# Kernel tuning notes

Measured on AMD Instinct MI355X. Metric: run time of the kernel, lower is better.

The kernel has to match this reference:

```python
import jax, jax.numpy as jnp
import numpy as np

T = 0.2          # temperature
W = 0.1          # loss weight
BIG = 2 ** 30    # sentinel label for masked-out samples


def setup_inputs() -> dict:
    key = jax.random.key(0)
    k1, k2, k3, k4 = jax.random.split(key, 4)
    bs, C, Gn, S = 32, 128, 256, 16
    grouped_features = jax.random.normal(k1, (bs, C, Gn, S), dtype=jnp.float32)
    # instance labels in [-1, 8): -1 = background
    proposal_instance_mask = jax.random.randint(k2, (bs, Gn, S), -1, 8, dtype=jnp.int32)
    # seed indices with duplicates possible (range 40 over 16 samples)
    grouped_indices = jax.random.randint(k3, (bs, Gn, S), 0, 40, dtype=jnp.int32)
    context_compen = jax.random.normal(k4, (1, C), dtype=jnp.float32)
    return {
        "proposal_instance_mask": proposal_instance_mask,
        "grouped_features": grouped_features,
        "grouped_indices": grouped_indices,
        "context_compen": context_compen,
    }


def _group_loss(feat, idx, lab, ctx):
    # feat: [S, C], idx: [S], lab: [S], ctx: [C]
    # NOTE: sum_{a,b} f_a . g_b / (n_f * n_g) == mean(f) . mean(g), so the
    # original tiny-mm contrastive loss reduces to pairwise dots of per-instance means.
    S, C = feat.shape
    pos = jnp.arange(S)
    # unique count of seed indices -> truncate to first u samples (as in torch code)
    si = jnp.sort(idx)
    u = 1 + jnp.sum(si[1:] != si[:-1])
    valid = pos < u
    lab_m = jnp.where(valid, lab, BIG)
    # per-group unique labels (sorted), jit-friendly
    sl = jnp.sort(lab_m)
    new = jnp.concatenate([jnp.ones((1,), bool), sl[1:] != sl[:-1]])
    cid = jnp.cumsum(new) - 1                      # compact id of each sorted label
    uniq = jnp.full((S,), BIG, sl.dtype).at[cid].set(sl)
    n_labels = jnp.sum(new & (sl != BIG))          # number of distinct valid labels
    has_bg = uniq[0] == -1                         # -1 sorts first if present
    # per-instance mean features via segment scatter-add
    comp = jnp.searchsorted(uniq, lab_m)           # sample -> compact instance slot
    sums = jnp.zeros((S, C), feat.dtype).at[comp].add(jnp.where(valid[:, None], feat, 0.0))
    cnts = jnp.zeros((S,), feat.dtype).at[comp].add(valid.astype(feat.dtype))
    means = sums / jnp.maximum(cnts, 1.0)[:, None]
    hb = has_bg.astype(jnp.int32)
    fg_count = n_labels - hb
    inst_num = fg_count + 1                        # bg slot always present
    # row 0 = bg mean (or context_compen if no bg), rows 1.. = fg means
    gidx = jnp.clip(pos + hb - 1, 0, S - 1)
    M = means[gidx]
    M = M.at[0].set(jnp.where(has_bg, M[0], ctx))
    inst_valid = pos < inst_num
    sim = (M @ M.T) / T                            # [S, S] tiny matmul of means
    sim_m = jnp.where(inst_valid[None, :], sim, -jnp.inf)
    lse = jax.scipy.special.logsumexp(sim_m, axis=1)
    li = lse - jnp.diagonal(sim)                   # -log(pos/(pos+neg)) per fg row
    fg_mask = inst_valid & (pos >= 1)
    gl = jnp.sum(jnp.where(fg_mask, li, 0.0)) / jnp.maximum(inst_num - 1, 1).astype(feat.dtype)
    return gl, fg_count >= 1


def reference(proposal_instance_mask, grouped_features, grouped_indices, context_compen):
    bs, C, Gn, S = grouped_features.shape
    feats = grouped_features.transpose(0, 2, 3, 1).reshape(-1, S, C)  # [G, S, C]
    idxs = grouped_indices.reshape(-1, S)
    labs = proposal_instance_mask.reshape(-1, S)
    ctx = context_compen[0]
    gl, gv = jax.vmap(lambda f, i, l: _group_loss(f, i, l, ctx))(feats, idxs, labs)
    gvf = gv.astype(gl.dtype)
    return jnp.sum(gl * gvf) / jnp.sum(gvf) * W
```

## Files before the change

### kernel.cpp

```cpp
#include <hip/hip_runtime.h>

#define GQ    8192
#define BLKG  8
#define MROW  132
#define SQRT5 2.23606797749978969f

template<int CTRL>
__device__ __forceinline__ float dpp_add(float v) {
    int t = __builtin_amdgcn_update_dpp(0, __float_as_int(v), CTRL, 0xF, 0xF, true);
    return v + __int_as_float(t);
}
__device__ __forceinline__ float wave_sum64(float v) {
    v = dpp_add<0x111>(v);
    v = dpp_add<0x112>(v);
    v = dpp_add<0x114>(v);
    v = dpp_add<0x118>(v);
    v = dpp_add<0x142>(v);
    v = dpp_add<0x143>(v);
    return v;
}

__global__ __launch_bounds__(64 * BLKG, 4) void group_loss_kernel(
    const int*   __restrict__ labs,
    const float* __restrict__ feats,
    const int*   __restrict__ idxs,
    const float* __restrict__ ctx,
    float2* __restrict__ ws)
{
    __shared__ float SH[128 * MROW];

    const int l  = threadIdx.x & 63;
    const int w  = threadIdx.x >> 6;
    const int g0 = blockIdx.x * BLKG;
    const int g  = g0 + w;
    const int b  = g0 >> 8;
    const int gn0 = g0 & 255;

    int myidx = -1, mylab = -2;
    if (l < 16) { myidx = idxs[g * 16 + l]; mylab = labs[g * 16 + l]; }
    const float cx0 = ctx[l], cx1 = ctx[l + 64];

    {
        const int half = l >> 5;
        const int lo   = l & 31;
        const float* base = feats + (long)b * 524288 + (long)gn0 * 16;
        #pragma unroll
        for (int k = 0; k < 8; ++k) {
            const int c = k * 16 + w * 2 + half;
            const float4 v = *(const float4*)(base + (long)c * 4096 + lo * 4);
            *(float4*)(SH + c * MROW + lo * 4) = v;
        }
    }
    __syncthreads();

    unsigned long long mm = ~0ull;
    #pragma unroll
    for (int bit = 0; bit < 6; ++bit) {
        const unsigned long long bb = __ballot((myidx >> bit) & 1);
        mm &= ((myidx >> bit) & 1) ? bb : ~bb;
    }
    const bool dup = (mm & ((1ull << l) - 1) & 0xFFFFull) != 0ull;
    const int u = __popcll(__ballot((l < 16) && !dup));

    const bool valid = l < u;
    const int bid = valid ? (mylab + 1) : 255;

    int cnt[9];
    #pragma unroll
    for (int r = 0; r < 9; ++r) cnt[r] = __popcll(__ballot(bid == r));
    const bool has_bg = cnt[0] > 0;
    int fg_count = 0, pm = 0;
    #pragma unroll
    for (int r = 1; r < 9; ++r)
        if (cnt[r] > 0) { ++fg_count; pm |= 1 << r; }

    float fa[16], fb[16];
    {
        const float* Ra = SH + l * MROW + w * 16;
        const float* Rb = SH + (l + 64) * MROW + w * 16;
        #pragma unroll
        for (int q = 0; q < 4; ++q) {
            const float4 x = *(const float4*)(Ra + 4 * q);
            const float4 y = *(const float4*)(Rb + 4 * q);
            fa[4*q+0] = x.x; fa[4*q+1] = x.y; fa[4*q+2] = x.z; fa[4*q+3] = x.w;
            fb[4*q+0] = y.x; fb[4*q+1] = y.y; fb[4*q+2] = y.z; fb[4*q+3] = y.w;
        }
    }

    float m0[9] = {0,0,0,0,0,0,0,0,0};
    float m1[9] = {0,0,0,0,0,0,0,0,0};
    #pragma unroll
    for (int s = 0; s < 16; ++s) {
        if (s < u) {
            const int bs = __builtin_amdgcn_readlane(bid, s);
            switch (bs) {
                case 0: m0[0] += fa[s]; m1[0] += fb[s]; break;
                case 1: m0[1] += fa[s]; m1[1] += fb[s]; break;
                case 2: m0[2] += fa[s]; m1[2] += fb[s]; break;
                case 3: m0[3] += fa[s]; m1[3] += fb[s]; break;
                case 4: m0[4] += fa[s]; m1[4] += fb[s]; break;
                case 5: m0[5] += fa[s]; m1[5] += fb[s]; break;
                case 6: m0[6] += fa[s]; m1[6] += fb[s]; break;
                case 7: m0[7] += fa[s]; m1[7] += fb[s]; break;
                case 8: m0[8] += fa[s]; m1[8] += fb[s]; break;
            }
        }
    }
    #pragma unroll
    for (int r = 0; r < 9; ++r) {
        const float sc = SQRT5 / (float)(cnt[r] > 0 ? cnt[r] : 1);
        m0[r] *= sc; m1[r] *= sc;
    }
    if (!has_bg) { m0[0] = cx0 * SQRT5; m1[0] = cx1 * SQRT5; }

    const int PI_[44] = {1,1, 2,2,2, 3,3,3,3, 4,4,4,4,4, 5,5,5,5,5,5,
                         6,6,6,6,6,6,6, 7,7,7,7,7,7,7,7, 8,8,8,8,8,8,8,8,8};
    const int PJ_[44] = {0,1, 0,1,2, 0,1,2,3, 0,1,2,3,4, 0,1,2,3,4,5,
                         0,1,2,3,4,5,6, 0,1,2,3,4,5,6,7, 0,1,2,3,4,5,6,7,8};
    const int cm = pm | 1;
    int svi[44];
    #pragma unroll
    for (int k = 0; k < 44; ++k) {
        float pv = m0[PI_[k]] * m0[PJ_[k]] + m1[PI_[k]] * m1[PJ_[k]];
        pv = wave_sum64(pv);
        const int s = __builtin_amdgcn_readlane(__float_as_int(pv), 63);
        const bool keep = (((cm >> PI_[k]) & 1) != 0) && (((cm >> PJ_[k]) & 1) != 0);
        svi[k] = keep ? s : 0xFF800000;
    }
    const int OFF_[9] = {0, 0, 2, 5, 9, 14, 20, 27, 35};
    #define SK(i, j) __int_as_float(svi[((i) >= (j)) ? (OFF_[(i)] + (j)) : (OFF_[(j)] + (i))])

    float ssum = 0.0f;
    #pragma unroll
    for (int r = 1; r < 9; ++r) {
        if ((pm >> r) & 1) {
            float vmax = SK(r, 0);
            #pragma unroll
            for (int j = 1; j < 9; ++j) vmax = fmaxf(vmax, SK(r, j));
            float se = 0.0f;
            #pragma unroll
            for (int j = 0; j < 9; ++j) se += __expf(SK(r, j) - vmax);
            ssum += vmax + __logf(se) - SK(r, r);
        }
    }
    #undef SK

    if (l == 0) {
        float2 r;
        r.x = ssum / (float)(fg_count > 0 ? fg_count : 1);
        r.y = (fg_count > 0) ? 1.0f : 0.0f;
        ws[g] = r;
    }
}

__global__ __launch_bounds__(1024) void reduce_kernel(
    const float2* __restrict__ ws, float* __restrict__ out)
{
    __shared__ float sa[1024], sb[1024];
    const int t = threadIdx.x;
    float a = 0.0f, b2 = 0.0f;
    for (int g = t; g < GQ; g += 1024) {
        float2 v = ws[g];
        a += v.x; b2 += v.y;
    }
    sa[t] = a; sb[t] = b2;
    __syncthreads();
    for (int off = 512; off > 0; off >>= 1) {
        if (t < off) { sa[t] += sa[t + off]; sb[t] += sb[t + off]; }
        __syncthreads();
    }
    if (t == 0) out[0] = 0.1f * (sa[0] / sb[0]);
}

extern "C" void kernel_launch(void* const* d_in, const int* in_sizes, int n_in,
                              void* d_out, int out_size, void* d_ws, size_t ws_size,
                              hipStream_t stream) {
    const int*   labs  = (const int*)d_in[0];
    const float* feats = (const float*)d_in[1];
    const int*   idxs  = (const int*)d_in[2];
    const float* ctx   = (const float*)d_in[3];
    float* out = (float*)d_out;
    float2* ws = (float2*)d_ws;

    group_loss_kernel<<<GQ / BLKG, 64 * BLKG, 0, stream>>>(labs, feats, idxs, ctx, ws);
    reduce_kernel<<<1, 1024, 0, stream>>>(ws, out);
}
```

Before: 115.1 us.

## Halve LDS staging with two-phase channel loads and butterfly-reduce similarity rows

Feature staging is split into two halves of 64 channels that reuse one half-sized LDS buffer, and the launch-bounds occupancy target is raised from 4 to 8 blocks. The 44 separate full-wave DPP reductions are replaced by a transpose-style butterfly shuffle reduction that builds the 9x9 similarity rows in LDS. The per-row log-sum-exp is then spread across lanes 1-8 and combined with a shuffle. The aim is higher occupancy and fewer reduction instructions, at the cost of extra barriers and serialising the two channel-load phases.

Result: faster. 110.0 us (-4.4%).

```diff
diff --git a/kernel.cpp b/kernel.cpp
--- a/kernel.cpp
+++ b/kernel.cpp
@@ -2,32 +2,20 @@
 
 #define GQ    8192
 #define BLKG  8
+#define NBLK  (GQ / BLKG)
 #define MROW  132
+#define STG   (64 * MROW)
+#define SIMW  72
 #define SQRT5 2.23606797749978969f
 
-template<int CTRL>
-__device__ __forceinline__ float dpp_add(float v) {
-    int t = __builtin_amdgcn_update_dpp(0, __float_as_int(v), CTRL, 0xF, 0xF, true);
-    return v + __int_as_float(t);
-}
-__device__ __forceinline__ float wave_sum64(float v) {
-    v = dpp_add<0x111>(v);
-    v = dpp_add<0x112>(v);
-    v = dpp_add<0x114>(v);
-    v = dpp_add<0x118>(v);
-    v = dpp_add<0x142>(v);
-    v = dpp_add<0x143>(v);
-    return v;
-}
-
-__global__ __launch_bounds__(64 * BLKG, 4) void group_loss_kernel(
+__global__ __launch_bounds__(64 * BLKG, 8) void group_loss_kernel(
     const int*   __restrict__ labs,
     const float* __restrict__ feats,
     const int*   __restrict__ idxs,
     const float* __restrict__ ctx,
-    float2* __restrict__ ws)
+    float2*      __restrict__ ws)
 {
-    __shared__ float SH[128 * MROW];
+    __shared__ float SH[STG + BLKG * SIMW];
 
     const int l  = threadIdx.x & 63;
     const int w  = threadIdx.x >> 6;
@@ -35,23 +23,21 @@
     const int g  = g0 + w;
     const int b  = g0 >> 8;
     const int gn0 = g0 & 255;
+    float* SIM = SH + STG + w * SIMW;
+
+    const float* base = feats + (long)b * 524288 + (long)gn0 * 16;
+    const int lo = l & 31;
 
     int myidx = -1, mylab = -2;
     if (l < 16) { myidx = idxs[g * 16 + l]; mylab = labs[g * 16 + l]; }
     const float cx0 = ctx[l], cx1 = ctx[l + 64];
 
-    {
-        const int half = l >> 5;
-        const int lo   = l & 31;
-        const float* base = feats + (long)b * 524288 + (long)gn0 * 16;
-        #pragma unroll
-        for (int k = 0; k < 8; ++k) {
-            const int c = k * 16 + w * 2 + half;
-            const float4 v = *(const float4*)(base + (long)c * 4096 + lo * 4);
-            *(float4*)(SH + c * MROW + lo * 4) = v;
-        }
-    }
-    __syncthreads();
+    #pragma unroll
+    for (int k = 0; k < 4; ++k) {
+        const int ch = w * 8 + k * 2 + (l >> 5);
+        const float4 v = *(const float4*)(base + (long)ch * 4096 + lo * 4);
+        *(float4*)(SH + ch * MROW + lo * 4) = v;
+    }
 
     unsigned long long mm = ~0ull;
     #pragma unroll
@@ -65,86 +51,145 @@
     const bool valid = l < u;
     const int bid = valid ? (mylab + 1) : 255;
 
-    int cnt[9];
-    #pragma unroll
-    for (int r = 0; r < 9; ++r) cnt[r] = __popcll(__ballot(bid == r));
-    const bool has_bg = cnt[0] > 0;
+    int cnt9[9];
+    #pragma unroll
+    for (int r = 0; r < 9; ++r) cnt9[r] = __popcll(__ballot(bid == r));
+    const bool has_bg = cnt9[0] > 0;
     int fg_count = 0, pm = 0;
     #pragma unroll
     for (int r = 1; r < 9; ++r)
-        if (cnt[r] > 0) { ++fg_count; pm |= 1 << r; }
-
-    float fa[16], fb[16];
-    {
-        const float* Ra = SH + l * MROW + w * 16;
-        const float* Rb = SH + (l + 64) * MROW + w * 16;
-        #pragma unroll
-        for (int q = 0; q < 4; ++q) {
-            const float4 x = *(const float4*)(Ra + 4 * q);
-            const float4 y = *(const float4*)(Rb + 4 * q);
-            fa[4*q+0] = x.x; fa[4*q+1] = x.y; fa[4*q+2] = x.z; fa[4*q+3] = x.w;
-            fb[4*q+0] = y.x; fb[4*q+1] = y.y; fb[4*q+2] = y.z; fb[4*q+3] = y.w;
-        }
-    }
+        if (cnt9[r] > 0) { ++fg_count; pm |= 1 << r; }
 
     float m0[9] = {0,0,0,0,0,0,0,0,0};
     float m1[9] = {0,0,0,0,0,0,0,0,0};
-    #pragma unroll
-    for (int s = 0; s < 16; ++s) {
-        if (s < u) {
-            const int bs = __builtin_amdgcn_readlane(bid, s);
-            switch (bs) {
-                case 0: m0[0] += fa[s]; m1[0] += fb[s]; break;
-                case 1: m0[1] += fa[s]; m1[1] += fb[s]; break;
-                case 2: m0[2] += fa[s]; m1[2] += fb[s]; break;
-                case 3: m0[3] += fa[s]; m1[3] += fb[s]; break;
-                case 4: m0[4] += fa[s]; m1[4] += fb[s]; break;
-                case 5: m0[5] += fa[s]; m1[5] += fb[s]; break;
-                case 6: m0[6] += fa[s]; m1[6] += fb[s]; break;
-                case 7: m0[7] += fa[s]; m1[7] += fb[s]; break;
-                case 8: m0[8] += fa[s]; m1[8] += fb[s]; break;
+
+    __syncthreads();
+    {
+        const float* R = SH + l * MROW + w * 16;
+        #pragma unroll
+        for (int q = 0; q < 4; ++q) {
+            const float4 x = *(const float4*)(R + 4 * q);
+            #pragma unroll
+            for (int e = 0; e < 4; ++e) {
+                const int s = 4 * q + e;
+                if (s < u) {
+                    const int bs = __builtin_amdgcn_readlane(bid, s);
+                    const float v = (e == 0) ? x.x : (e == 1) ? x.y
+                                  : (e == 2) ? x.z : x.w;
+                    switch (bs) {
+                        case 0: m0[0] += v; break;  case 1: m0[1] += v; break;
+                        case 2: m0[2] += v; break;  case 3: m0[3] += v; break;
+                        case 4: m0[4] += v; break;  case 5: m0[5] += v; break;
+                        case 6: m0[6] += v; break;  case 7: m0[7] += v; break;
+                        case 8: m0[8] += v; break;
+                    }
+                }
             }
         }
     }
+    __syncthreads();
+
+    #pragma unroll
+    for (int k = 0; k < 4; ++k) {
+        const int ch = w * 8 + k * 2 + (l >> 5);
+        const float4 v = *(const float4*)(base + (long)(64 + ch) * 4096 + lo * 4);
+        *(float4*)(SH + ch * MROW + lo * 4) = v;
+    }
+    __syncthreads();
+
+    {
+        const float* R = SH + l * MROW + w * 16;
+        #pragma unroll
+        for (int q = 0; q < 4; ++q) {
+            const float4 x = *(const float4*)(R + 4 * q);
+            #pragma unroll
+            for (int e = 0; e < 4; ++e) {
+                const int s = 4 * q + e;
+                if (s < u) {
+                    const int bs = __builtin_amdgcn_readlane(bid, s);
+                    const float v = (e == 0) ? x.x : (e == 1) ? x.y
+                                  : (e == 2) ? x.z : x.w;
+                    switch (bs) {
+                        case 0: m1[0] += v; break;  case 1: m1[1] += v; break;
+                        case 2: m1[2] += v; break;  case 3: m1[3] += v; break;
+                        case 4: m1[4] += v; break;  case 5: m1[5] += v; break;
+                        case 6: m1[6] += v; break;  case 7: m1[7] += v; break;
+                        case 8: m1[8] += v; break;
+                    }
+                }
+            }
+        }
+    }
+
     #pragma unroll
     for (int r = 0; r < 9; ++r) {
-        const float sc = SQRT5 / (float)(cnt[r] > 0 ? cnt[r] : 1);
+        const float sc = SQRT5 / (float)(cnt9[r] > 0 ? cnt9[r] : 1);
         m0[r] *= sc; m1[r] *= sc;
     }
     if (!has_bg) { m0[0] = cx0 * SQRT5; m1[0] = cx1 * SQRT5; }
 
-    const int PI_[44] = {1,1, 2,2,2, 3,3,3,3, 4,4,4,4,4, 5,5,5,5,5,5,
-                         6,6,6,6,6,6,6, 7,7,7,7,7,7,7,7, 8,8,8,8,8,8,8,8,8};
-    const int PJ_[44] = {0,1, 0,1,2, 0,1,2,3, 0,1,2,3,4, 0,1,2,3,4,5,
-                         0,1,2,3,4,5,6, 0,1,2,3,4,5,6,7, 0,1,2,3,4,5,6,7,8};
+    #pragma unroll
+    for (int r = 1; r <= 8; ++r) {
+        float p[8];
+        #pragma unroll
+        for (int j = 0; j < 8; ++j)
+            p[j] = m0[r] * m0[j] + m1[r] * m1[j];
+        #pragma unroll
+        for (int i = 0; i < 4; ++i) {
+            const float send = (l & 32) ? p[i] : p[i + 4];
+            const float recv = __shfl_xor(send, 32);
+            p[i] = ((l & 32) ? p[i + 4] : p[i]) + recv;
+        }
+        #pragma unroll
+        for (int i = 0; i < 2; ++i) {
+            const float send = (l & 16) ? p[i] : p[i + 2];
+            const float recv = __shfl_xor(send, 16);
+            p[i] = ((l & 16) ? p[i + 2] : p[i]) + recv;
+        }
+        {
+            const float send = (l & 8) ? p[0] : p[1];
+            const float recv = __shfl_xor(send, 8);
+            p[0] = ((l & 8) ? p[1] : p[0]) + recv;
+        }
+        p[0] += __shfl_xor(p[0], 4);
+        p[0] += __shfl_xor(p[0], 2);
+        p[0] += __shfl_xor(p[0], 1);
+        if ((l & 7) == 0) SIM[(r - 1) * 8 + (l >> 3)] = p[0];
+    }
+    float s88 = m0[8] * m0[8] + m1[8] * m1[8];
+    s88 += __shfl_xor(s88, 1);  s88 += __shfl_xor(s88, 2);
+    s88 += __shfl_xor(s88, 4);  s88 += __shfl_xor(s88, 8);
+    s88 += __shfl_xor(s88, 16); s88 += __shfl_xor(s88, 32);
+
     const int cm = pm | 1;
-    int svi[44];
-    #pragma unroll
-    for (int k = 0; k < 44; ++k) {
-        float pv = m0[PI_[k]] * m0[PJ_[k]] + m1[PI_[k]] * m1[PJ_[k]];
-        pv = wave_sum64(pv);
-        const int s = __builtin_amdgcn_readlane(__float_as_int(pv), 63);
-        const bool keep = (((cm >> PI_[k]) & 1) != 0) && (((cm >> PJ_[k]) & 1) != 0);
-        svi[k] = keep ? s : 0xFF800000;
-    }
-    const int OFF_[9] = {0, 0, 2, 5, 9, 14, 20, 27, 35};
-    #define SK(i, j) __int_as_float(svi[((i) >= (j)) ? (OFF_[(i)] + (j)) : (OFF_[(j)] + (i))])
-
-    float ssum = 0.0f;
-    #pragma unroll
-    for (int r = 1; r < 9; ++r) {
-        if ((pm >> r) & 1) {
-            float vmax = SK(r, 0);
-            #pragma unroll
-            for (int j = 1; j < 9; ++j) vmax = fmaxf(vmax, SK(r, j));
-            float se = 0.0f;
-            #pragma unroll
-            for (int j = 0; j < 9; ++j) se += __expf(SK(r, j) - vmax);
-            ssum += vmax + __logf(se) - SK(r, r);
-        }
-    }
-    #undef SK
-
+    const float NINF = __int_as_float(0xFF800000);
+    float li = 0.0f;
+    if (l >= 1 && l <= 8) {
+        const float* Rw = SIM + (l - 1) * 8;
+        const float4 ra = *(const float4*)(Rw);
+        const float4 rb = *(const float4*)(Rw + 4);
+        const float s8 = SIM[56 + l];
+        float srow[9] = { ra.x, ra.y, ra.z, ra.w, rb.x, rb.y, rb.z, rb.w,
+                          (l == 8) ? s88 : s8 };
+        float vmax = NINF, diag = 0.0f, v[9];
+        #pragma unroll
+        for (int j = 0; j < 9; ++j) {
+            v[j] = ((cm >> j) & 1) ? srow[j] : NINF;
+            vmax = fmaxf(vmax, v[j]);
+            if (j >= 1) diag = (l == j) ? srow[j] : diag;
+        }
+        float se = 0.0f;
+        #pragma unroll
+        for (int j = 0; j < 9; ++j) se += __expf(v[j] - vmax);
+        li = vmax + __logf(se) - diag;
+        li = ((pm >> l) & 1) ? li : 0.0f;
+    }
+
+    float ssum = li;
+    ssum += __shfl_down(ssum, 8);
+    ssum += __shfl_down(ssum, 4);
+    ssum += __shfl_down(ssum, 2);
+    ssum += __shfl_down(ssum, 1);
     if (l == 0) {
         float2 r;
         r.x = ssum / (float)(fg_count > 0 ? fg_count : 1);
@@ -182,6 +227,6 @@
     float* out = (float*)d_out;
     float2* ws = (float2*)d_ws;
 
-    group_loss_kernel<<<GQ / BLKG, 64 * BLKG, 0, stream>>>(labs, feats, idxs, ctx, ws);
+    group_loss_kernel<<<NBLK, 64 * BLKG, 0, stream>>>(labs, feats, idxs, ctx, ws);
     reduce_kernel<<<1, 1024, 0, stream>>>(ws, out);
 }
```
